# Optimization experiments

Measured on AMD Instinct MI355X. Metric: run time of the kernel, lower is better.

Reference implementation:

```python
import jax, jax.numpy as jnp
import numpy as np

HEADS = 8
DIM_HEAD = 64
WINDOW = 256
CAUSAL = True


def _sliding_window_mask(seq_len: int, window: int, causal: bool) -> jnp.ndarray:
    i = jnp.arange(seq_len)[:, None]
    j = jnp.arange(seq_len)[None, :]
    # attend iff i - window + 1 <= j <= i + window - 1 (end_pos exclusive)
    mask = (j >= i - window + 1) & (j <= i + window - 1)
    if causal:
        mask = mask & (j <= i)
    return mask  # (S, S) bool


def setup_inputs() -> dict:
    key = jax.random.key(0)
    k1, k2, k3 = jax.random.split(key, 3)
    dim = 512
    inner = HEADS * DIM_HEAD
    x = jax.random.normal(k1, (2, 2048, dim), dtype=jnp.float32)
    W_qkv = jax.random.normal(k2, (dim, 3 * inner), dtype=jnp.float32) * 0.02
    W_out = jax.random.normal(k3, (inner, dim), dtype=jnp.float32) * 0.02
    return {"x": x, "W_qkv": W_qkv, "W_out": W_out}


def reference(x, W_qkv, W_out):
    B, S, D = x.shape
    H, Dh = HEADS, DIM_HEAD
    scale = Dh ** (-0.5)
    qkv = x @ W_qkv  # (B, S, 3*H*Dh)
    q, k, v = jnp.split(qkv, 3, axis=-1)
    q = q.reshape(B, S, H, Dh).transpose(0, 2, 1, 3)  # (B, H, S, Dh)
    k = k.reshape(B, S, H, Dh).transpose(0, 2, 1, 3)
    v = v.reshape(B, S, H, Dh).transpose(0, 2, 1, 3)
    scores = jnp.einsum('bhid,bhjd->bhij', q, k) * scale
    mask = _sliding_window_mask(S, WINDOW, CAUSAL)
    mask_value = -jnp.finfo(scores.dtype).max
    scores = jnp.where(mask[None, None, :, :], scores, mask_value)
    attn = jax.nn.softmax(scores, axis=-1)  # (B, H, S, S)
    out = jnp.einsum('bhij,bhjd->bhid', attn, v)
    out = out.transpose(0, 2, 1, 3).reshape(B, S, H * Dh)
    out = out @ W_out  # (B, S, D)
    return (out, attn)
```

## Files before the change

### kernel.cpp

```cpp
#include <hip/hip_runtime.h>
#include <hip/hip_bf16.h>

typedef __bf16 bf16x8 __attribute__((ext_vector_type(8)));
typedef __bf16 bf16x4 __attribute__((ext_vector_type(4)));
typedef float f32x4 __attribute__((ext_vector_type(4)));

#define MFMA16(a,b,c) __builtin_amdgcn_mfma_f32_16x16x32_bf16(a, b, c, 0, 0, 0)

__device__ inline void fill_attn_rows(float* __restrict__ attn, int rowStart, int rowEnd,
                                      int tid) {
  const f32x4 z4 = {0.f, 0.f, 0.f, 0.f};
  for (int g = rowStart; g < rowEnd; g++) {
    const int bh = g >> 11, i = g & 2047;
    const int qt = i >> 6;
    const int lo = qt >= 4 ? (qt - 4) << 6 : 0;
    const int hi = (qt + 1) << 6;
    float* rp = attn + ((size_t)bh << 22) + ((size_t)i << 11);
    for (int j = tid << 2; j < lo; j += 1024)
      __builtin_nontemporal_store(z4, reinterpret_cast<f32x4*>(rp + j));
    for (int j = hi + (tid << 2); j < 2048; j += 1024)
      __builtin_nontemporal_store(z4, reinterpret_cast<f32x4*>(rp + j));
  }
}

__device__ inline void fill_block_chunk(float* __restrict__ attn, int fillStart, int fillEnd,
                                        int fid, int nfill, int tid) {
  const int total = fillEnd - fillStart;
  const int per = (total + nfill - 1) / nfill;
  const int myStart = fillStart + fid * per;
  int myEnd = myStart + per;
  if (myEnd > fillEnd) myEnd = fillEnd;
  if (myStart < myEnd) fill_attn_rows(attn, myStart, myEnd, tid);
}

__device__ inline void transpose_body(const float* __restrict__ in, __bf16* __restrict__ out,
                                      int R, int C, int tile, int tid, float (*t)[65]) {
  const int tilesC = C >> 6;
  const int tc = tile % tilesC, tr = tile / tilesC;
  const int r0 = tr << 6, c0 = tc << 6;
  const int ri = tid >> 2, cq = (tid & 3) << 4;
#pragma unroll
  for (int e = 0; e < 16; e += 4) {
    float4 v = *reinterpret_cast<const float4*>(&in[(size_t)(r0 + ri) * C + c0 + cq + e]);
    t[ri][cq + e]     = v.x;
    t[ri][cq + e + 1] = v.y;
    t[ri][cq + e + 2] = v.z;
    t[ri][cq + e + 3] = v.w;
  }
  __syncthreads();
  const int co = tid >> 2, rq = (tid & 3) << 4;
  __attribute__((aligned(16))) __bf16 buf[16];
#pragma unroll
  for (int e = 0; e < 16; e++) buf[e] = (__bf16)t[rq + e][co];
  *reinterpret_cast<bf16x8*>(&out[(size_t)(c0 + co) * R + r0 + rq])     = *reinterpret_cast<bf16x8*>(&buf[0]);
  *reinterpret_cast<bf16x8*>(&out[(size_t)(c0 + co) * R + r0 + rq + 8]) = *reinterpret_cast<bf16x8*>(&buf[8]);
}

__global__ __launch_bounds__(256) void prep(const float* __restrict__ x,
                                            const float* __restrict__ Wqkv,
                                            const float* __restrict__ Wout,
                                            __bf16* __restrict__ Xb,
                                            __bf16* __restrict__ Wqt,
                                            __bf16* __restrict__ Wot) {
  __shared__ float t[64][65];
  const int bid = blockIdx.x, tid = threadIdx.x;
  if (bid < 2048) {
    const int i = (bid * 256 + tid) * 4;
    float4 v = *reinterpret_cast<const float4*>(x + i);
    bf16x4 o;
    o[0] = (__bf16)v.x; o[1] = (__bf16)v.y; o[2] = (__bf16)v.z; o[3] = (__bf16)v.w;
    *reinterpret_cast<bf16x4*>(Xb + i) = o;
  } else if (bid < 2240) {
    transpose_body(Wqkv, Wqt, 512, 1536, bid - 2048, tid, t);
  } else {
    transpose_body(Wout, Wot, 512, 512, bid - 2240, tid, t);
  }
}

template <typename OT>
__global__ __launch_bounds__(256) void gemm_bt(const __bf16* __restrict__ A,
                                               const __bf16* __restrict__ Bt,
                                               OT* __restrict__ C, int M, int N, int K,
                                               float* __restrict__ fillAttn,
                                               int fillStart, int fillEnd, int gxCompute) {
  __shared__ __bf16 As[128][72];
  __shared__ __bf16 Bs[128][72];
  const int tid = threadIdx.x;

  if ((int)blockIdx.x >= gxCompute) {
    const int nfx = gridDim.x - gxCompute;
    const int fid = (blockIdx.x - gxCompute) + nfx * blockIdx.y;
    fill_block_chunk(fillAttn, fillStart, fillEnd, fid, nfx * gridDim.y, tid);
    return;
  }

  const int wave = tid >> 6, lane = tid & 63;
  const int c = lane & 15, q4 = lane >> 4;
  const int bm = blockIdx.y << 7, bn = blockIdx.x << 7;
  const int wm = (wave >> 1) << 6, wn = (wave & 1) << 6;
  f32x4 acc[4][4];
#pragma unroll
  for (int m = 0; m < 4; m++)
#pragma unroll
    for (int n = 0; n < 4; n++)
#pragma unroll
      for (int e = 0; e < 4; e++) acc[m][n][e] = 0.f;

  const int srow = tid >> 1, scol = (tid & 1) << 5;
  for (int k0 = 0; k0 < K; k0 += 64) {
    __syncthreads();
    const __bf16* ag = A + (size_t)(bm + srow) * K + k0 + scol;
    const __bf16* bg = Bt + (size_t)(bn + srow) * K + k0 + scol;
    bf16x8 av[4], bv[4];
#pragma unroll
    for (int r = 0; r < 4; r++) av[r] = *reinterpret_cast<const bf16x8*>(ag + r * 8);
#pragma unroll
    for (int r = 0; r < 4; r++) bv[r] = *reinterpret_cast<const bf16x8*>(bg + r * 8);
#pragma unroll
    for (int r = 0; r < 4; r++) *reinterpret_cast<bf16x8*>(&As[srow][scol + r * 8]) = av[r];
#pragma unroll
    for (int r = 0; r < 4; r++) *reinterpret_cast<bf16x8*>(&Bs[srow][scol + r * 8]) = bv[r];
    __syncthreads();
#pragma unroll
    for (int ks = 0; ks < 2; ks++) {
      const int kk = ks * 32 + q4 * 8;
      bf16x8 af[4], bfv[4];
#pragma unroll
      for (int m = 0; m < 4; m++) af[m] = *reinterpret_cast<const bf16x8*>(&As[wm + m * 16 + c][kk]);
#pragma unroll
      for (int n = 0; n < 4; n++) bfv[n] = *reinterpret_cast<const bf16x8*>(&Bs[wn + n * 16 + c][kk]);
#pragma unroll
      for (int m = 0; m < 4; m++)
#pragma unroll
        for (int n = 0; n < 4; n++) acc[m][n] = MFMA16(af[m], bfv[n], acc[m][n]);
    }
  }
#pragma unroll
  for (int m = 0; m < 4; m++)
#pragma unroll
    for (int n = 0; n < 4; n++)
#pragma unroll
      for (int r2 = 0; r2 < 4; r2++) {
        const int row = bm + wm + m * 16 + q4 * 4 + r2;
        const int col = bn + wn + n * 16 + c;
        C[(size_t)row * N + col] = (OT)acc[m][n][r2];
      }
}

__global__ __launch_bounds__(256) void attn_fused(const __bf16* __restrict__ QKV,
                                                  float* __restrict__ attn,
                                                  __bf16* __restrict__ AO) {
  __shared__ __bf16 Qs[64][72];
  __shared__ __bf16 Ks[64][72];
  __shared__ __bf16 Ps[64][72];
  __shared__ float red[4][64];
  __shared__ float rowstat[64];
  const int tid = threadIdx.x;

  if (blockIdx.x >= 32) {
    const int fid = (blockIdx.x - 32) + (gridDim.x - 32) * blockIdx.y;
    fill_block_chunk(attn, 16000, 24000, fid, (gridDim.x - 32) * gridDim.y, tid);
    return;
  }

  const int qt = blockIdx.x, bh = blockIdx.y;
  const int b = bh >> 3, h = bh & 7;
  const int qi0 = qt << 6;
  const int wave = tid >> 6, lane = tid & 63;
  const int c = lane & 15, q4 = lane >> 4;

  {
    const int r = tid >> 2, qq = (tid & 3) << 4;
    const __bf16* src = QKV + (size_t)(b * 2048 + qi0 + r) * 1536 + h * 64 + qq;
    bf16x8 v0 = *reinterpret_cast<const bf16x8*>(src);
    bf16x8 v1 = *reinterpret_cast<const bf16x8*>(src + 8);
    *reinterpret_cast<bf16x8*>(&Qs[r][qq]) = v0;
    *reinterpret_cast<bf16x8*>(&Qs[r][qq + 8]) = v1;
  }

  f32x4 acc[5][4];
#pragma unroll
  for (int t = 0; t < 5; t++)
#pragma unroll
    for (int m = 0; m < 4; m++)
#pragma unroll
      for (int e = 0; e < 4; e++) acc[t][m][e] = 0.f;

#pragma unroll
  for (int t = 0; t < 5; t++) {
    const int jt0 = (qt - 4 + t) << 6;
    if (jt0 < 0) continue;
    __syncthreads();
    {
      const int r = tid >> 2, qq = (tid & 3) << 4;
      const __bf16* src = QKV + (size_t)(b * 2048 + jt0 + r) * 1536 + 512 + h * 64 + qq;
      bf16x8 v0 = *reinterpret_cast<const bf16x8*>(src);
      bf16x8 v1 = *reinterpret_cast<const bf16x8*>(src + 8);
      *reinterpret_cast<bf16x8*>(&Ks[r][qq]) = v0;
      *reinterpret_cast<bf16x8*>(&Ks[r][qq + 8]) = v1;
    }
    __syncthreads();
#pragma unroll
    for (int ks = 0; ks < 2; ks++) {
      const int kk = ks * 32 + q4 * 8;
      bf16x8 bfr = *reinterpret_cast<const bf16x8*>(&Ks[wave * 16 + c][kk]);
#pragma unroll
      for (int m = 0; m < 4; m++) {
        bf16x8 afr = *reinterpret_cast<const bf16x8*>(&Qs[m * 16 + c][kk]);
        acc[t][m] = MFMA16(afr, bfr, acc[t][m]);
      }
    }
  }

  const float scale = 0.125f;
#pragma unroll
  for (int t = 0; t < 5; t++) {
    const int jb = ((qt - 4 + t) << 6) + wave * 16 + c;
#pragma unroll
    for (int m = 0; m < 4; m++)
#pragma unroll
      for (int r2 = 0; r2 < 4; r2++) {
        const int ig = qi0 + m * 16 + q4 * 4 + r2;
        const bool valid = (jb >= 0) && (jb <= ig) && (jb >= ig - 255);
        acc[t][m][r2] = valid ? acc[t][m][r2] * scale : -1e30f;
      }
  }

  float pm[16];
#pragma unroll
  for (int m = 0; m < 4; m++)
#pragma unroll
    for (int r2 = 0; r2 < 4; r2++) {
      float v = acc[0][m][r2];
#pragma unroll
      for (int t = 1; t < 5; t++) v = fmaxf(v, acc[t][m][r2]);
      pm[m * 4 + r2] = v;
    }
#pragma unroll
  for (int off = 8; off >= 1; off >>= 1)
#pragma unroll
    for (int i = 0; i < 16; i++) pm[i] = fmaxf(pm[i], __shfl_xor(pm[i], off, 64));
  if (c == 0) {
#pragma unroll
    for (int m = 0; m < 4; m++)
#pragma unroll
      for (int r2 = 0; r2 < 4; r2++) red[wave][m * 16 + q4 * 4 + r2] = pm[m * 4 + r2];
  }
  __syncthreads();
  if (tid < 64)
    rowstat[tid] = fmaxf(fmaxf(red[0][tid], red[1][tid]), fmaxf(red[2][tid], red[3][tid]));
  __syncthreads();

  float rmax[16], ps[16];
#pragma unroll
  for (int m = 0; m < 4; m++)
#pragma unroll
    for (int r2 = 0; r2 < 4; r2++) {
      rmax[m * 4 + r2] = rowstat[m * 16 + q4 * 4 + r2];
      ps[m * 4 + r2] = 0.f;
    }
#pragma unroll
  for (int t = 0; t < 5; t++)
#pragma unroll
    for (int m = 0; m < 4; m++)
#pragma unroll
      for (int r2 = 0; r2 < 4; r2++) {
        float p = __expf(acc[t][m][r2] - rmax[m * 4 + r2]);
        acc[t][m][r2] = p;
        ps[m * 4 + r2] += p;
      }
#pragma unroll
  for (int off = 8; off >= 1; off >>= 1)
#pragma unroll
    for (int i = 0; i < 16; i++) ps[i] += __shfl_xor(ps[i], off, 64);
  if (c == 0) {
#pragma unroll
    for (int m = 0; m < 4; m++)
#pragma unroll
      for (int r2 = 0; r2 < 4; r2++) red[wave][m * 16 + q4 * 4 + r2] = ps[m * 4 + r2];
  }
  __syncthreads();
  if (tid < 64) rowstat[tid] = red[0][tid] + red[1][tid] + red[2][tid] + red[3][tid];
  __syncthreads();

#pragma unroll
  for (int m = 0; m < 4; m++)
#pragma unroll
    for (int r2 = 0; r2 < 4; r2++) {
      const float rinv = 1.0f / rowstat[m * 16 + q4 * 4 + r2];
#pragma unroll
      for (int t = 0; t < 5; t++) acc[t][m][r2] *= rinv;
    }

  f32x4 o[4];
#pragma unroll
  for (int n = 0; n < 4; n++)
#pragma unroll
    for (int e = 0; e < 4; e++) o[n][e] = 0.f;

#pragma unroll
  for (int t = 0; t < 5; t++) {
    const int jt0 = (qt - 4 + t) << 6;
    if (jt0 < 0) continue;
    __syncthreads();
#pragma unroll
    for (int m = 0; m < 4; m++)
#pragma unroll
      for (int r2 = 0; r2 < 4; r2++)
        Ps[m * 16 + q4 * 4 + r2][wave * 16 + c] = (__bf16)acc[t][m][r2];
    {
      const int j = tid >> 2, dq = tid & 3;
#pragma unroll
      for (int r = 0; r < 2; r++) {
        const int d0 = (dq + r * 4) << 3;
        bf16x8 v = *reinterpret_cast<const bf16x8*>(
            QKV + (size_t)(b * 2048 + jt0 + j) * 1536 + 1024 + h * 64 + d0);
#pragma unroll
        for (int e = 0; e < 8; e++) Ks[d0 + e][j] = v[e];
      }
    }
    __syncthreads();
#pragma unroll
    for (int ks = 0; ks < 2; ks++) {
      const int kk = ks * 32 + q4 * 8;
      bf16x8 af = *reinterpret_cast<const bf16x8*>(&Ps[wave * 16 + c][kk]);
#pragma unroll
      for (int n = 0; n < 4; n++) {
        bf16x8 bfr = *reinterpret_cast<const bf16x8*>(&Ks[n * 16 + c][kk]);
        o[n] = MFMA16(af, bfr, o[n]);
      }
    }
  }

#pragma unroll
  for (int n = 0; n < 4; n++)
#pragma unroll
    for (int r2 = 0; r2 < 4; r2++) {
      const int i = qi0 + wave * 16 + q4 * 4 + r2;
      const int d = n * 16 + c;
      AO[(size_t)(b * 2048 + i) * 512 + h * 64 + d] = (__bf16)o[n][r2];
    }

  float* arow = attn + ((size_t)bh << 22);
#pragma unroll
  for (int t = 0; t < 5; t++) {
    const int jt0 = (qt - 4 + t) << 6;
    if (jt0 < 0) continue;
    const int jb = jt0 + wave * 16 + c;
#pragma unroll
    for (int m = 0; m < 4; m++)
#pragma unroll
      for (int r2 = 0; r2 < 4; r2++) {
        const int ig = qi0 + m * 16 + q4 * 4 + r2;
        arow[(size_t)ig * 2048 + jb] = acc[t][m][r2];
      }
  }
}

extern "C" void kernel_launch(void* const* d_in, const int* in_sizes, int n_in,
                              void* d_out, int out_size, void* d_ws, size_t ws_size,
                              hipStream_t stream) {
  const float* x = (const float*)d_in[0];
  const float* Wqkv = (const float*)d_in[1];
  const float* Wout = (const float*)d_in[2];
  float* out = (float*)d_out;
  float* attn = out + (size_t)2 * 2048 * 512;

  char* ws = (char*)d_ws;
  __bf16* Xb   = (__bf16*)(ws);
  __bf16* Wqt  = (__bf16*)(ws + 4194304);
  __bf16* Wot  = (__bf16*)(ws + 4194304 + 1572864);
  __bf16* QKVb = (__bf16*)(ws + 4194304 + 1572864 + 524288);
  __bf16* AOb  = (__bf16*)(ws + 4194304 + 1572864 + 524288 + 12582912);

  prep<<<2304, 256, 0, stream>>>(x, Wqkv, Wout, Xb, Wqt, Wot);

  gemm_bt<__bf16><<<dim3(24, 32), 256, 0, stream>>>(Xb, Wqt, QKVb, 4096, 1536, 512,
                                                    attn, 0, 16000, 12);

  attn_fused<<<dim3(48, 16), 256, 0, stream>>>(QKVb, attn, AOb);

  gemm_bt<float><<<dim3(12, 32), 256, 0, stream>>>(AOb, Wot, out, 4096, 512, 512,
                                                   attn, 24000, 32768, 4);
}
```

Before: 90.76 us.

## Fuse x bf16 cast into QKV GEMM and prefetch tiles in GEMM and attention

Removes the separate x-to-bf16 conversion pass from the prep kernel and converts fp32 x to bf16 inside the QKV GEMM's global load. Both GEMMs now prefetch the next K tile into registers while the current tile is computed. The attention kernel double-buffers its K, V and P shared tiles and prefetches the next K/V tile into registers, which removes one barrier per iteration. This cuts a full read and write of x and hides global load latency, at the cost of more registers and shared memory and reading twice as many bytes of A in the QKV GEMM.

```diff
diff --git a/kernel.cpp b/kernel.cpp
--- a/kernel.cpp
+++ b/kernel.cpp
@@ -56,29 +56,18 @@
   *reinterpret_cast<bf16x8*>(&out[(size_t)(c0 + co) * R + r0 + rq + 8]) = *reinterpret_cast<bf16x8*>(&buf[8]);
 }
 
-__global__ __launch_bounds__(256) void prep(const float* __restrict__ x,
-                                            const float* __restrict__ Wqkv,
+__global__ __launch_bounds__(256) void prep(const float* __restrict__ Wqkv,
                                             const float* __restrict__ Wout,
-                                            __bf16* __restrict__ Xb,
                                             __bf16* __restrict__ Wqt,
                                             __bf16* __restrict__ Wot) {
   __shared__ float t[64][65];
   const int bid = blockIdx.x, tid = threadIdx.x;
-  if (bid < 2048) {
-    const int i = (bid * 256 + tid) * 4;
-    float4 v = *reinterpret_cast<const float4*>(x + i);
-    bf16x4 o;
-    o[0] = (__bf16)v.x; o[1] = (__bf16)v.y; o[2] = (__bf16)v.z; o[3] = (__bf16)v.w;
-    *reinterpret_cast<bf16x4*>(Xb + i) = o;
-  } else if (bid < 2240) {
-    transpose_body(Wqkv, Wqt, 512, 1536, bid - 2048, tid, t);
-  } else {
-    transpose_body(Wout, Wot, 512, 512, bid - 2240, tid, t);
-  }
-}
-
-template <typename OT>
-__global__ __launch_bounds__(256) void gemm_bt(const __bf16* __restrict__ A,
+  if (bid < 192) transpose_body(Wqkv, Wqt, 512, 1536, bid, tid, t);
+  else           transpose_body(Wout, Wot, 512, 512, bid - 192, tid, t);
+}
+
+template <typename AT, typename OT>
+__global__ __launch_bounds__(256) void gemm_bt(const AT* __restrict__ A,
                                                const __bf16* __restrict__ Bt,
                                                OT* __restrict__ C, int M, int N, int K,
                                                float* __restrict__ fillAttn,
@@ -107,20 +96,40 @@
       for (int e = 0; e < 4; e++) acc[m][n][e] = 0.f;
 
   const int srow = tid >> 1, scol = (tid & 1) << 5;
+  bf16x8 av[4], bv[4];
+
+  auto loadA = [&](int k0) {
+    const AT* ag = A + (size_t)(bm + srow) * K + k0 + scol;
+    if constexpr (sizeof(AT) == 4) {
+#pragma unroll
+      for (int r = 0; r < 4; r++) {
+        float4 lo = *reinterpret_cast<const float4*>(ag + r * 8);
+        float4 hi = *reinterpret_cast<const float4*>(ag + r * 8 + 4);
+        bf16x8 v;
+        v[0] = (__bf16)lo.x; v[1] = (__bf16)lo.y; v[2] = (__bf16)lo.z; v[3] = (__bf16)lo.w;
+        v[4] = (__bf16)hi.x; v[5] = (__bf16)hi.y; v[6] = (__bf16)hi.z; v[7] = (__bf16)hi.w;
+        av[r] = v;
+      }
+    } else {
+#pragma unroll
+      for (int r = 0; r < 4; r++) av[r] = *reinterpret_cast<const bf16x8*>(ag + r * 8);
+    }
+  };
+  auto loadB = [&](int k0) {
+    const __bf16* bg = Bt + (size_t)(bn + srow) * K + k0 + scol;
+#pragma unroll
+    for (int r = 0; r < 4; r++) bv[r] = *reinterpret_cast<const bf16x8*>(bg + r * 8);
+  };
+
+  loadA(0); loadB(0);
   for (int k0 = 0; k0 < K; k0 += 64) {
     __syncthreads();
-    const __bf16* ag = A + (size_t)(bm + srow) * K + k0 + scol;
-    const __bf16* bg = Bt + (size_t)(bn + srow) * K + k0 + scol;
-    bf16x8 av[4], bv[4];
-#pragma unroll
-    for (int r = 0; r < 4; r++) av[r] = *reinterpret_cast<const bf16x8*>(ag + r * 8);
-#pragma unroll
-    for (int r = 0; r < 4; r++) bv[r] = *reinterpret_cast<const bf16x8*>(bg + r * 8);
 #pragma unroll
     for (int r = 0; r < 4; r++) *reinterpret_cast<bf16x8*>(&As[srow][scol + r * 8]) = av[r];
 #pragma unroll
     for (int r = 0; r < 4; r++) *reinterpret_cast<bf16x8*>(&Bs[srow][scol + r * 8]) = bv[r];
     __syncthreads();
+    if (k0 + 64 < K) { loadA(k0 + 64); loadB(k0 + 64); }
 #pragma unroll
     for (int ks = 0; ks < 2; ks++) {
       const int kk = ks * 32 + q4 * 8;
@@ -151,8 +160,8 @@
                                                   float* __restrict__ attn,
                                                   __bf16* __restrict__ AO) {
   __shared__ __bf16 Qs[64][72];
-  __shared__ __bf16 Ks[64][72];
-  __shared__ __bf16 Ps[64][72];
+  __shared__ __bf16 Ks[2][64][72];
+  __shared__ __bf16 Ps[2][64][72];
   __shared__ float red[4][64];
   __shared__ float rowstat[64];
   const int tid = threadIdx.x;
@@ -168,14 +177,13 @@
   const int qi0 = qt << 6;
   const int wave = tid >> 6, lane = tid & 63;
   const int c = lane & 15, q4 = lane >> 4;
+  const int base = b * 2048;
+  const int r = tid >> 2, qq = (tid & 3) << 4;
 
   {
-    const int r = tid >> 2, qq = (tid & 3) << 4;
-    const __bf16* src = QKV + (size_t)(b * 2048 + qi0 + r) * 1536 + h * 64 + qq;
-    bf16x8 v0 = *reinterpret_cast<const bf16x8*>(src);
-    bf16x8 v1 = *reinterpret_cast<const bf16x8*>(src + 8);
-    *reinterpret_cast<bf16x8*>(&Qs[r][qq]) = v0;
-    *reinterpret_cast<bf16x8*>(&Qs[r][qq + 8]) = v1;
+    const __bf16* src = QKV + (size_t)(base + qi0 + r) * 1536 + h * 64 + qq;
+    *reinterpret_cast<bf16x8*>(&Qs[r][qq]) = *reinterpret_cast<const bf16x8*>(src);
+    *reinterpret_cast<bf16x8*>(&Qs[r][qq + 8]) = *reinterpret_cast<const bf16x8*>(src + 8);
   }
 
   f32x4 acc[5][4];
@@ -186,30 +194,36 @@
 #pragma unroll
       for (int e = 0; e < 4; e++) acc[t][m][e] = 0.f;
 
+  const int tfirst = qt >= 4 ? 0 : 4 - qt;
+  bf16x8 kv0, kv1;
+  {
+    const __bf16* s = QKV + (size_t)(base + ((qt - 4 + tfirst) << 6) + r) * 1536 + 512 + h * 64 + qq;
+    kv0 = *reinterpret_cast<const bf16x8*>(s);
+    kv1 = *reinterpret_cast<const bf16x8*>(s + 8);
+  }
+  int cur = 0;
 #pragma unroll
   for (int t = 0; t < 5; t++) {
-    const int jt0 = (qt - 4 + t) << 6;
-    if (jt0 < 0) continue;
-    __syncthreads();
-    {
-      const int r = tid >> 2, qq = (tid & 3) << 4;
-      const __bf16* src = QKV + (size_t)(b * 2048 + jt0 + r) * 1536 + 512 + h * 64 + qq;
-      bf16x8 v0 = *reinterpret_cast<const bf16x8*>(src);
-      bf16x8 v1 = *reinterpret_cast<const bf16x8*>(src + 8);
-      *reinterpret_cast<bf16x8*>(&Ks[r][qq]) = v0;
-      *reinterpret_cast<bf16x8*>(&Ks[r][qq + 8]) = v1;
+    if (qt - 4 + t < 0) continue;
+    *reinterpret_cast<bf16x8*>(&Ks[cur][r][qq]) = kv0;
+    *reinterpret_cast<bf16x8*>(&Ks[cur][r][qq + 8]) = kv1;
+    if (t < 4) {
+      const __bf16* s = QKV + (size_t)(base + ((qt - 3 + t) << 6) + r) * 1536 + 512 + h * 64 + qq;
+      kv0 = *reinterpret_cast<const bf16x8*>(s);
+      kv1 = *reinterpret_cast<const bf16x8*>(s + 8);
     }
     __syncthreads();
 #pragma unroll
     for (int ks = 0; ks < 2; ks++) {
       const int kk = ks * 32 + q4 * 8;
-      bf16x8 bfr = *reinterpret_cast<const bf16x8*>(&Ks[wave * 16 + c][kk]);
+      bf16x8 bfr = *reinterpret_cast<const bf16x8*>(&Ks[cur][wave * 16 + c][kk]);
 #pragma unroll
       for (int m = 0; m < 4; m++) {
         bf16x8 afr = *reinterpret_cast<const bf16x8*>(&Qs[m * 16 + c][kk]);
         acc[t][m] = MFMA16(afr, bfr, acc[t][m]);
       }
     }
+    cur ^= 1;
   }
 
   const float scale = 0.125f;
@@ -298,38 +312,44 @@
 #pragma unroll
     for (int e = 0; e < 4; e++) o[n][e] = 0.f;
 
+  const int jv = tid >> 2, dqa = tid & 3;
+  bf16x8 vr0, vr1;
+  {
+    const __bf16* s = QKV + (size_t)(base + ((qt - 4 + tfirst) << 6) + jv) * 1536 + 1024 + h * 64;
+    vr0 = *reinterpret_cast<const bf16x8*>(s + dqa * 8);
+    vr1 = *reinterpret_cast<const bf16x8*>(s + (dqa + 4) * 8);
+  }
+  int pcur = 0;
 #pragma unroll
   for (int t = 0; t < 5; t++) {
-    const int jt0 = (qt - 4 + t) << 6;
-    if (jt0 < 0) continue;
-    __syncthreads();
+    if (qt - 4 + t < 0) continue;
 #pragma unroll
     for (int m = 0; m < 4; m++)
 #pragma unroll
       for (int r2 = 0; r2 < 4; r2++)
-        Ps[m * 16 + q4 * 4 + r2][wave * 16 + c] = (__bf16)acc[t][m][r2];
-    {
-      const int j = tid >> 2, dq = tid & 3;
-#pragma unroll
-      for (int r = 0; r < 2; r++) {
-        const int d0 = (dq + r * 4) << 3;
-        bf16x8 v = *reinterpret_cast<const bf16x8*>(
-            QKV + (size_t)(b * 2048 + jt0 + j) * 1536 + 1024 + h * 64 + d0);
-#pragma unroll
-        for (int e = 0; e < 8; e++) Ks[d0 + e][j] = v[e];
-      }
+        Ps[pcur][m * 16 + q4 * 4 + r2][wave * 16 + c] = (__bf16)acc[t][m][r2];
+#pragma unroll
+    for (int e = 0; e < 8; e++) {
+      Ks[pcur][dqa * 8 + e][jv] = vr0[e];
+      Ks[pcur][(dqa + 4) * 8 + e][jv] = vr1[e];
+    }
+    if (t < 4) {
+      const __bf16* s = QKV + (size_t)(base + ((qt - 3 + t) << 6) + jv) * 1536 + 1024 + h * 64;
+      vr0 = *reinterpret_cast<const bf16x8*>(s + dqa * 8);
+      vr1 = *reinterpret_cast<const bf16x8*>(s + (dqa + 4) * 8);
     }
     __syncthreads();
 #pragma unroll
     for (int ks = 0; ks < 2; ks++) {
       const int kk = ks * 32 + q4 * 8;
-      bf16x8 af = *reinterpret_cast<const bf16x8*>(&Ps[wave * 16 + c][kk]);
+      bf16x8 af = *reinterpret_cast<const bf16x8*>(&Ps[pcur][wave * 16 + c][kk]);
 #pragma unroll
       for (int n = 0; n < 4; n++) {
-        bf16x8 bfr = *reinterpret_cast<const bf16x8*>(&Ks[n * 16 + c][kk]);
+        bf16x8 bfr = *reinterpret_cast<const bf16x8*>(&Ks[pcur][n * 16 + c][kk]);
         o[n] = MFMA16(af, bfr, o[n]);
       }
     }
+    pcur ^= 1;
   }
 
 #pragma unroll
@@ -338,7 +358,7 @@
     for (int r2 = 0; r2 < 4; r2++) {
       const int i = qi0 + wave * 16 + q4 * 4 + r2;
       const int d = n * 16 + c;
-      AO[(size_t)(b * 2048 + i) * 512 + h * 64 + d] = (__bf16)o[n][r2];
+      AO[(size_t)(base + i) * 512 + h * 64 + d] = (__bf16)o[n][r2];
     }
 
   float* arow = attn + ((size_t)bh << 22);
@@ -367,19 +387,18 @@
   float* attn = out + (size_t)2 * 2048 * 512;
 
   char* ws = (char*)d_ws;
-  __bf16* Xb   = (__bf16*)(ws);
-  __bf16* Wqt  = (__bf16*)(ws + 4194304);
-  __bf16* Wot  = (__bf16*)(ws + 4194304 + 1572864);
-  __bf16* QKVb = (__bf16*)(ws + 4194304 + 1572864 + 524288);
-  __bf16* AOb  = (__bf16*)(ws + 4194304 + 1572864 + 524288 + 12582912);
-
-  prep<<<2304, 256, 0, stream>>>(x, Wqkv, Wout, Xb, Wqt, Wot);
-
-  gemm_bt<__bf16><<<dim3(24, 32), 256, 0, stream>>>(Xb, Wqt, QKVb, 4096, 1536, 512,
-                                                    attn, 0, 16000, 12);
+  __bf16* Wqt  = (__bf16*)(ws);
+  __bf16* Wot  = (__bf16*)(ws + 1572864);
+  __bf16* QKVb = (__bf16*)(ws + 1572864 + 524288);
+  __bf16* AOb  = (__bf16*)(ws + 1572864 + 524288 + 12582912);
+
+  prep<<<256, 256, 0, stream>>>(Wqkv, Wout, Wqt, Wot);
+
+  gemm_bt<float, __bf16><<<dim3(24, 32), 256, 0, stream>>>(x, Wqt, QKVb, 4096, 1536, 512,
+                                                           attn, 0, 16000, 12);
 
   attn_fused<<<dim3(48, 16), 256, 0, stream>>>(QKVb, attn, AOb);
 
-  gemm_bt<float><<<dim3(12, 32), 256, 0, stream>>>(AOb, Wot, out, 4096, 512, 512,
-                                                   attn, 24000, 32768, 4);
-}
+  gemm_bt<__bf16, float><<<dim3(12, 32), 256, 0, stream>>>(AOb, Wot, out, 4096, 512, 512,
+                                                           attn, 24000, 32768, 4);
+}
```

New measurement: 88.66 us. 1.02x faster.
